# Kernel tuning notes

Measured on AMD Instinct MI355X. Metric: run time of the kernel, lower is better.

Reference implementation:

```python
import jax, jax.numpy as jnp
import numpy as np

# Static multi-scale feature map shapes (value_spatial_shapes) - constants for jit.
SPATIAL = [(128, 128), (64, 64), (32, 32), (16, 16)]
D = 256      # embed_dim
NH = 8       # num_heads
HD = D // NH # head_dim = 32
L = 4        # num_levels
P = 4        # num_points
TP = NH * L * P  # 128 total points


def setup_inputs() -> dict:
    key = jax.random.key(0)
    ks = jax.random.split(key, 10)
    bs, lq = 8, 300
    lv = sum(h * w for h, w in SPATIAL)  # 21760
    s = D ** -0.5
    return {
        "query": jax.random.normal(ks[0], (bs, lq, D), jnp.float32),
        "reference_points": jax.random.uniform(ks[1], (bs, lq, L, 4), jnp.float32),
        "value": jax.random.normal(ks[2], (bs, lv, D), jnp.float32),
        "W_value": jax.random.normal(ks[3], (D, D), jnp.float32) * s,
        "b_value": jnp.zeros((D,), jnp.float32),
        "W_off": jax.random.normal(ks[4], (D, TP * 2), jnp.float32) * (s * 0.01),
        "b_off": jax.random.normal(ks[5], (TP * 2,), jnp.float32) * 0.5,
        "W_attn": jax.random.normal(ks[6], (D, TP), jnp.float32) * (s * 0.01),
        "b_attn": jnp.zeros((TP,), jnp.float32),
        "W_out": jax.random.normal(ks[7], (D, D), jnp.float32) * s,
        "b_out": jnp.zeros((D,), jnp.float32),
    }


def _grid_sample(img, grid):
    """torch F.grid_sample(mode='bilinear', padding_mode='zeros', align_corners=False).
    img: [N, C, H, W]; grid: [N, Hg, Wg, 2] in [-1, 1] (x, y). Returns [N, C, Hg, Wg]."""
    N, C, H, W = img.shape
    gx = (grid[..., 0] + 1.0) * (W * 0.5) - 0.5
    gy = (grid[..., 1] + 1.0) * (H * 0.5) - 0.5
    x0f = jnp.floor(gx)
    y0f = jnp.floor(gy)
    x0 = x0f.astype(jnp.int32)
    y0 = y0f.astype(jnp.int32)
    x1, y1 = x0 + 1, y0 + 1
    wx1 = gx - x0f
    wy1 = gy - y0f
    wx0 = 1.0 - wx1
    wy0 = 1.0 - wy1
    imgf = img.reshape(N, C, H * W)

    def gather(ix, iy):
        valid = (ix >= 0) & (ix < W) & (iy >= 0) & (iy < H)
        idx = jnp.clip(iy, 0, H - 1) * W + jnp.clip(ix, 0, W - 1)
        v = jax.vmap(lambda im, ii: im[:, ii])(imgf, idx)  # [N, C, Hg, Wg]
        return v * valid[:, None, :, :].astype(img.dtype)

    return (gather(x0, y0) * (wx0 * wy0)[:, None]
            + gather(x1, y0) * (wx1 * wy0)[:, None]
            + gather(x0, y1) * (wx0 * wy1)[:, None]
            + gather(x1, y1) * (wx1 * wy1)[:, None])


def reference(query, reference_points, value, W_value, b_value, W_off, b_off,
              W_attn, b_attn, W_out, b_out):
    bs, lq, _ = query.shape
    # value projection + head split
    v = (value @ W_value + b_value).reshape(bs, -1, NH, HD)
    # sampling offsets and attention weights from query
    off = (query @ W_off + b_off).reshape(bs, lq, NH, L, P, 2)
    aw = jax.nn.softmax((query @ W_attn + b_attn).reshape(bs, lq, NH, L * P), axis=-1)
    aw = aw.reshape(bs, lq, NH, L, P)
    # reference_points last dim == 4 branch (cx, cy, w, h)
    ref = reference_points  # [bs, lq, L, 4]
    loc = ref[:, :, None, :, None, :2] + off / P * ref[:, :, None, :, None, 2:] * 0.5
    grids = 2.0 * loc - 1.0  # [bs, lq, NH, L, P, 2]
    # split value per level
    splits = np.cumsum([h * w for h, w in SPATIAL])[:-1]
    v_list = jnp.split(v, splits, axis=1)
    samples = []
    for l, (h, w) in enumerate(SPATIAL):
        img = v_list[l].transpose(0, 2, 3, 1).reshape(bs * NH, HD, h, w)
        g = grids[:, :, :, l].transpose(0, 2, 1, 3, 4).reshape(bs * NH, lq, P, 2)
        samples.append(_grid_sample(img, g))  # [bs*NH, HD, lq, P]
    samp = jnp.stack(samples, axis=-2).reshape(bs * NH, HD, lq, L * P)
    awr = aw.transpose(0, 2, 1, 3, 4).reshape(bs * NH, 1, lq, L * P)
    out = (samp * awr).sum(-1).reshape(bs, NH * HD, lq).transpose(0, 2, 1)
    return out @ W_out + b_out
```

## Files before the change

kernel.cpp:

```cpp
#include <hip/hip_runtime.h>
#include <hip/hip_bf16.h>

typedef short bf16x8 __attribute__((ext_vector_type(8)));
typedef unsigned short u16x8 __attribute__((ext_vector_type(8)));
typedef float f32x4 __attribute__((ext_vector_type(4)));

#define LQ 300
#define LV 21760
#define NQ 2400
#define MROWS 174080

#define VBM 16
#define VGRID 512
#define QBLK 38
#define VNT (MROWS / VBM)

__device__ __forceinline__ unsigned short f2bf(float x) {
    __hip_bfloat16 h = __float2bfloat16(x);
    return *reinterpret_cast<unsigned short*>(&h);
}
__device__ __forceinline__ float bf2f(unsigned short s) {
    return __uint_as_float(((unsigned)s) << 16);
}
__device__ __forceinline__ bf16x8 cvt8(float4 a, float4 b) {
    u16x8 u;
    u[0] = f2bf(a.x); u[1] = f2bf(a.y); u[2] = f2bf(a.z); u[3] = f2bf(a.w);
    u[4] = f2bf(b.x); u[5] = f2bf(b.y); u[6] = f2bf(b.z); u[7] = f2bf(b.w);
    return (bf16x8)u;
}
__device__ __forceinline__ bf16x8 cvt8v(f32x4 a, f32x4 b) {
    u16x8 u;
    u[0] = f2bf(a[0]); u[1] = f2bf(a[1]); u[2] = f2bf(a[2]); u[3] = f2bf(a[3]);
    u[4] = f2bf(b[0]); u[5] = f2bf(b[1]); u[6] = f2bf(b[2]); u[7] = f2bf(b[3]);
    return (bf16x8)u;
}

__global__ void k_wt(const float* __restrict__ Wv, const float* __restrict__ Woff,
                     const float* __restrict__ Wattn, const float* __restrict__ Wout,
                     unsigned short* __restrict__ ws) {
    int i = blockIdx.x * 256 + threadIdx.x;
    if (i < 65536) {
        int n = i >> 8, k = i & 255;
        ws[i] = f2bf(Wv[k * 256 + n]);
    } else if (i < 65536 + 98304) {
        int j = i - 65536;
        int n = j >> 8, k = j & 255;
        float s = (n < 256) ? Woff[k * 256 + n] : Wattn[k * 128 + (n - 256)];
        ws[i] = f2bf(s);
    } else {
        int j = i - 163840;
        int n = j >> 8, k = j & 255;
        ws[i] = f2bf(Wout[k * 256 + n]);
    }
}

__global__ __launch_bounds__(256, 2) void k_vgemm(
    const float* __restrict__ A, const unsigned short* __restrict__ Bt,
    const float* __restrict__ bias, unsigned short* __restrict__ V,
    const float* __restrict__ Q, const unsigned short* __restrict__ Woa,
    const float* __restrict__ b_off, const float* __restrict__ b_attn,
    float* __restrict__ offattn)
{
    __shared__ __align__(16) float buf[4][VBM * 256];
    const int t = threadIdx.x;
    const int lane = t & 63;
    const int wv = t >> 6;
    const int fr = lane & 15, kg = lane >> 4;

    if (blockIdx.x < QBLK) {
        const int rowBase = blockIdx.x * 64;
        int rr[4];
#pragma unroll
        for (int m = 0; m < 4; ++m) rr[m] = min(rowBase + m * 16 + fr, NQ - 1);

        f32x4 acc[4][6];
#pragma unroll
        for (int m = 0; m < 4; m++)
#pragma unroll
            for (int n = 0; n < 6; n++) { f32x4 z = {0.f, 0.f, 0.f, 0.f}; acc[m][n] = z; }

#pragma unroll
        for (int kk = 0; kk < 8; ++kk) {
            const int kb = kk * 32 + kg * 8;
            bf16x8 a[4];
#pragma unroll
            for (int m = 0; m < 4; ++m) {
                float4 q0 = *(const float4*)(Q + (size_t)rr[m] * 256 + kb);
                float4 q1 = *(const float4*)(Q + (size_t)rr[m] * 256 + kb + 4);
                a[m] = cvt8(q0, q1);
            }
#pragma unroll
            for (int n = 0; n < 6; n++) {
                bf16x8 bb = *(const bf16x8*)(Woa + (size_t)(wv * 96 + n * 16 + fr) * 256 + kb);
#pragma unroll
                for (int m = 0; m < 4; ++m)
                    acc[m][n] = __builtin_amdgcn_mfma_f32_16x16x32_bf16(a[m], bb, acc[m][n], 0, 0, 0);
            }
        }

#pragma unroll
        for (int m = 0; m < 4; m++) {
#pragma unroll
            for (int n = 0; n < 6; n++) {
                int col = wv * 96 + n * 16 + fr;
                float bvv = (col < 256) ? b_off[col] : b_attn[col - 256];
#pragma unroll
                for (int r = 0; r < 4; r++) {
                    int row = rowBase + m * 16 + kg * 4 + r;
                    if (row < NQ) offattn[(size_t)row * 384 + col] = acc[m][n][r] + bvv;
                }
            }
        }
        return;
    }

    bf16x8 bw[8][4];
#pragma unroll
    for (int kk = 0; kk < 8; ++kk)
#pragma unroll
        for (int n = 0; n < 4; ++n)
            bw[kk][n] = *(const bf16x8*)(Bt + (size_t)(wv * 64 + n * 16 + fr) * 256 + kk * 32 + kg * 8);
    float bv[4];
#pragma unroll
    for (int n = 0; n < 4; ++n) bv[n] = bias[wv * 64 + n * 16 + fr];

#define VSTAGE(tile, cb)                                                                  \
    {                                                                                     \
        const char* tb = (const char*)(A + (size_t)(tile) * (VBM * 256));                 \
        _Pragma("unroll")                                                                 \
        for (int i = 0; i < 4; ++i) {                                                     \
            const int r = wv * 4 + i;                                                     \
            __builtin_amdgcn_global_load_lds(                                             \
                (const __attribute__((address_space(1))) void*)                           \
                    (tb + (size_t)r * 1024 + ((lane * 16) ^ ((r & 7) << 4))),             \
                (__attribute__((address_space(3))) void*)&buf[cb][r * 256], 16, 0, 0);    \
        }                                                                                 \
    }

    const int tb0 = (int)blockIdx.x - QBLK;
    VSTAGE(tb0, 0);
    if (tb0 + VGRID < VNT)     VSTAGE(tb0 + VGRID, 1);
    if (tb0 + 2 * VGRID < VNT) VSTAGE(tb0 + 2 * VGRID, 2);

    int cur = 0;
    for (int tile = tb0; tile < VNT; tile += VGRID, cur = (cur + 1) & 3) {
        const int nxt3 = tile + 3 * VGRID;
        if (nxt3 < VNT) VSTAGE(nxt3, (cur + 3) & 3);
        int a = (tile + VGRID < VNT) + (tile + 2 * VGRID < VNT) + (nxt3 < VNT);
        if (a == 3)      asm volatile("s_waitcnt vmcnt(12)" ::: "memory");
        else if (a == 2) asm volatile("s_waitcnt vmcnt(8)" ::: "memory");
        else if (a == 1) asm volatile("s_waitcnt vmcnt(4)" ::: "memory");
        else             asm volatile("s_waitcnt vmcnt(0)" ::: "memory");
        __builtin_amdgcn_s_barrier();

        const float* lp = buf[cur];
        f32x4 acc[4];
#pragma unroll
        for (int n = 0; n < 4; ++n) { f32x4 z = {0.f, 0.f, 0.f, 0.f}; acc[n] = z; }

#pragma unroll
        for (int kk = 0; kk < 8; ++kk) {
            const int bsw = ((kk * 32 + kg * 8) * 4) ^ ((fr & 7) << 4);
            f32x4 af0 = *(const f32x4*)((const char*)(lp + fr * 256) + bsw);
            f32x4 af1 = *(const f32x4*)((const char*)(lp + fr * 256) + (bsw ^ 16));
            bf16x8 aa = cvt8v(af0, af1);
#pragma unroll
            for (int n = 0; n < 4; ++n)
                acc[n] = __builtin_amdgcn_mfma_f32_16x16x32_bf16(aa, bw[kk][n], acc[n], 0, 0, 0);
        }

        __builtin_amdgcn_s_barrier();

        unsigned short* cp = (unsigned short*)buf[cur];
#pragma unroll
        for (int n = 0; n < 4; ++n)
#pragma unroll
            for (int r = 0; r < 4; ++r)
                cp[(kg * 4 + r) * 264 + wv * 64 + n * 16 + fr] = f2bf(acc[n][r] + bv[n]);
        asm volatile("s_waitcnt lgkmcnt(0)" ::: "memory");
        __builtin_amdgcn_sched_barrier(0);
        __builtin_amdgcn_s_barrier();

        unsigned short* ob = V + (size_t)tile * (VBM * 256);
#pragma unroll
        for (int i = 0; i < 2; ++i) {
            const int f = i * 256 + t;
            const int row = f >> 5, col = (f & 31) * 8;
            *(u16x8*)(ob + row * 256 + col) = *(const u16x8*)&cp[row * 264 + col];
        }
        __builtin_amdgcn_s_barrier();
    }
#undef VSTAGE
}

__global__ __launch_bounds__(256) void k_sample(
    const float* __restrict__ refp, const float* __restrict__ offattn,
    const unsigned short* __restrict__ V, unsigned short* __restrict__ att)
{
    __shared__ float aw[2][128], gx[2][128], gy[2][128];
    const int t = threadIdx.x;
    const int jj = t >> 7;
    const int tt = t & 127;
    const int row = blockIdx.x * 2 + jj;
    const int b = row / LQ;
    const float* oa = offattn + (size_t)row * 384;

    {
        float logit = oa[256 + tt];
        float m = logit;
        m = fmaxf(m, __shfl_xor(m, 1));
        m = fmaxf(m, __shfl_xor(m, 2));
        m = fmaxf(m, __shfl_xor(m, 4));
        m = fmaxf(m, __shfl_xor(m, 8));
        float e = __expf(logit - m);
        float s = e;
        s += __shfl_xor(s, 1);
        s += __shfl_xor(s, 2);
        s += __shfl_xor(s, 4);
        s += __shfl_xor(s, 8);
        aw[jj][tt] = e / s;
        const int l = (tt >> 2) & 3;
        const float Wl = (l == 0) ? 128.f : (l == 1) ? 64.f : (l == 2) ? 32.f : 16.f;
        float ox = oa[2 * tt], oy = oa[2 * tt + 1];
        const float* rp = refp + ((size_t)row * 4 + l) * 4;
        gx[jj][tt] = (rp[0] + ox * 0.125f * rp[2]) * Wl - 0.5f;
        gy[jj][tt] = (rp[1] + oy * 0.125f * rp[3]) * Wl - 0.5f;
    }
    __syncthreads();

    const int h = tt >> 4;
    const int ch = h * 32 + (tt & 15) * 2;
    float acc0 = 0.f, acc1 = 0.f;
#pragma unroll 4
    for (int p = 0; p < 16; p++) {
        const int l = p >> 2;
        const int Wl = (l == 0) ? 128 : (l == 1) ? 64 : (l == 2) ? 32 : 16;
        const int S  = (l == 0) ? 0 : (l == 1) ? 16384 : (l == 2) ? 20480 : 21504;
        int pt = h * 16 + p;
        float a  = aw[jj][pt];
        float sx = gx[jj][pt], sy = gy[jj][pt];
        float x0f = floorf(sx), y0f = floorf(sy);
        int   x0 = (int)x0f, y0 = (int)y0f;
        float wx1 = sx - x0f, wy1 = sy - y0f;
        float wx0 = 1.f - wx1, wy0 = 1.f - wy1;
        bool vx0 = (unsigned)x0 < (unsigned)Wl;
        bool vx1 = (unsigned)(x0 + 1) < (unsigned)Wl;
        bool vy0 = (unsigned)y0 < (unsigned)Wl;
        bool vy1 = (unsigned)(y0 + 1) < (unsigned)Wl;
        float p00x = 0.f, p00y = 0.f, p01x = 0.f, p01y = 0.f;
        float p10x = 0.f, p10y = 0.f, p11x = 0.f, p11y = 0.f;
        size_t pixBase = (size_t)b * LV + S;
        if (vy0) {
            size_t rb = (pixBase + (size_t)y0 * Wl) * 256 + ch;
            if (vx0) { unsigned u = *(const unsigned*)(V + rb + (size_t)x0 * 256);
                       p00x = bf2f((unsigned short)u); p00y = bf2f((unsigned short)(u >> 16)); }
            if (vx1) { unsigned u = *(const unsigned*)(V + rb + (size_t)x0 * 256 + 256);
                       p01x = bf2f((unsigned short)u); p01y = bf2f((unsigned short)(u >> 16)); }
        }
        if (vy1) {
            size_t rb = (pixBase + (size_t)(y0 + 1) * Wl) * 256 + ch;
            if (vx0) { unsigned u = *(const unsigned*)(V + rb + (size_t)x0 * 256);
                       p10x = bf2f((unsigned short)u); p10y = bf2f((unsigned short)(u >> 16)); }
            if (vx1) { unsigned u = *(const unsigned*)(V + rb + (size_t)x0 * 256 + 256);
                       p11x = bf2f((unsigned short)u); p11y = bf2f((unsigned short)(u >> 16)); }
        }
        acc0 += a * (wy0 * (wx0 * p00x + wx1 * p01x) + wy1 * (wx0 * p10x + wx1 * p11x));
        acc1 += a * (wy0 * (wx0 * p00y + wx1 * p01y) + wy1 * (wx0 * p10y + wx1 * p11y));
    }
    unsigned short o2[2] = { f2bf(acc0), f2bf(acc1) };
    *(unsigned*)(att + (size_t)row * 256 + ch) = *(const unsigned*)o2;
}

__global__ __launch_bounds__(256) void k_outproj(
    const unsigned short* __restrict__ att, const unsigned short* __restrict__ Wout,
    const float* __restrict__ b_out, float* __restrict__ out)
{
    const int t = threadIdx.x;
    const int lane = t & 63;
    const int wc = t >> 6;
    const int fr = lane & 15, kg = lane >> 4;
    const int rowBase = blockIdx.x * 64;

    f32x4 acc[4][4];
#pragma unroll
    for (int m = 0; m < 4; m++)
#pragma unroll
        for (int n = 0; n < 4; n++) { f32x4 z = {0.f, 0.f, 0.f, 0.f}; acc[m][n] = z; }

#pragma unroll
    for (int kk = 0; kk < 8; ++kk) {
        const int kb = kk * 32 + kg * 8;
        bf16x8 a[4], bb[4];
#pragma unroll
        for (int m = 0; m < 4; m++) {
            int row = min(rowBase + m * 16 + fr, NQ - 1);
            a[m] = *(const bf16x8*)(att + (size_t)row * 256 + kb);
        }
#pragma unroll
        for (int n = 0; n < 4; n++)
            bb[n] = *(const bf16x8*)(Wout + (size_t)(wc * 64 + n * 16 + fr) * 256 + kb);
#pragma unroll
        for (int m = 0; m < 4; m++)
#pragma unroll
            for (int n = 0; n < 4; n++)
                acc[m][n] = __builtin_amdgcn_mfma_f32_16x16x32_bf16(a[m], bb[n], acc[m][n], 0, 0, 0);
    }

#pragma unroll
    for (int m = 0; m < 4; m++) {
#pragma unroll
        for (int n = 0; n < 4; n++) {
            int col = wc * 64 + n * 16 + fr;
            float bvv = b_out[col];
#pragma unroll
            for (int r = 0; r < 4; r++) {
                int row = rowBase + m * 16 + kg * 4 + r;
                if (row < NQ) out[(size_t)row * 256 + col] = acc[m][n][r] + bvv;
            }
        }
    }
}

extern "C" void kernel_launch(void* const* d_in, const int* in_sizes, int n_in,
                              void* d_out, int out_size, void* d_ws, size_t ws_size,
                              hipStream_t stream) {
    const float* query   = (const float*)d_in[0];
    const float* refp    = (const float*)d_in[1];
    const float* value   = (const float*)d_in[2];
    const float* W_value = (const float*)d_in[3];
    const float* b_value = (const float*)d_in[4];
    const float* W_off   = (const float*)d_in[5];
    const float* b_off   = (const float*)d_in[6];
    const float* W_attn  = (const float*)d_in[7];
    const float* b_attn  = (const float*)d_in[8];
    const float* W_out   = (const float*)d_in[9];
    const float* b_out   = (const float*)d_in[10];
    float* out = (float*)d_out;

    unsigned short* wsu   = (unsigned short*)d_ws;
    unsigned short* Wt_v  = wsu;
    unsigned short* Wt_oa = Wt_v + 65536;
    unsigned short* Wt_out= Wt_oa + 98304;
    unsigned short* V     = Wt_out + 65536;
    float* offattn = (float*)(V + (size_t)MROWS * 256);
    unsigned short* att = (unsigned short*)(offattn + (size_t)NQ * 384);

    k_wt<<<896, 256, 0, stream>>>(W_value, W_off, W_attn, W_out, wsu);
    k_vgemm<<<VGRID + QBLK, 256, 0, stream>>>(value, Wt_v, b_value, V,
                                              query, Wt_oa, b_off, b_attn, offattn);
    k_sample<<<NQ / 2, 256, 0, stream>>>(refp, offattn, V, att);
    k_outproj<<<38, 256, 0, stream>>>(att, Wt_out, b_out, out);
}
```

Baseline: 114.6 us.

## Replace LDS-staged value GEMM pipeline with direct register prefetch per wave

```diff
diff --git a/kernel.cpp b/kernel.cpp
--- a/kernel.cpp
+++ b/kernel.cpp
@@ -26,12 +26,6 @@
     u16x8 u;
     u[0] = f2bf(a.x); u[1] = f2bf(a.y); u[2] = f2bf(a.z); u[3] = f2bf(a.w);
     u[4] = f2bf(b.x); u[5] = f2bf(b.y); u[6] = f2bf(b.z); u[7] = f2bf(b.w);
-    return (bf16x8)u;
-}
-__device__ __forceinline__ bf16x8 cvt8v(f32x4 a, f32x4 b) {
-    u16x8 u;
-    u[0] = f2bf(a[0]); u[1] = f2bf(a[1]); u[2] = f2bf(a[2]); u[3] = f2bf(a[3]);
-    u[4] = f2bf(b[0]); u[5] = f2bf(b[1]); u[6] = f2bf(b[2]); u[7] = f2bf(b[3]);
     return (bf16x8)u;
 }
 
@@ -61,7 +55,7 @@
     const float* __restrict__ b_off, const float* __restrict__ b_attn,
     float* __restrict__ offattn)
 {
-    __shared__ __align__(16) float buf[4][VBM * 256];
+    __shared__ unsigned short cscr[4][16 * 68];
     const int t = threadIdx.x;
     const int lane = t & 63;
     const int wv = t >> 6;
@@ -124,73 +118,59 @@
 #pragma unroll
     for (int n = 0; n < 4; ++n) bv[n] = bias[wv * 64 + n * 16 + fr];
 
-#define VSTAGE(tile, cb)                                                                  \
-    {                                                                                     \
-        const char* tb = (const char*)(A + (size_t)(tile) * (VBM * 256));                 \
-        _Pragma("unroll")                                                                 \
-        for (int i = 0; i < 4; ++i) {                                                     \
-            const int r = wv * 4 + i;                                                     \
-            __builtin_amdgcn_global_load_lds(                                             \
-                (const __attribute__((address_space(1))) void*)                           \
-                    (tb + (size_t)r * 1024 + ((lane * 16) ^ ((r & 7) << 4))),             \
-                (__attribute__((address_space(3))) void*)&buf[cb][r * 256], 16, 0, 0);    \
-        }                                                                                 \
-    }
-
+    unsigned short* scr = cscr[wv];
     const int tb0 = (int)blockIdx.x - QBLK;
-    VSTAGE(tb0, 0);
-    if (tb0 + VGRID < VNT)     VSTAGE(tb0 + VGRID, 1);
-    if (tb0 + 2 * VGRID < VNT) VSTAGE(tb0 + 2 * VGRID, 2);
-
-    int cur = 0;
-    for (int tile = tb0; tile < VNT; tile += VGRID, cur = (cur + 1) & 3) {
-        const int nxt3 = tile + 3 * VGRID;
-        if (nxt3 < VNT) VSTAGE(nxt3, (cur + 3) & 3);
-        int a = (tile + VGRID < VNT) + (tile + 2 * VGRID < VNT) + (nxt3 < VNT);
-        if (a == 3)      asm volatile("s_waitcnt vmcnt(12)" ::: "memory");
-        else if (a == 2) asm volatile("s_waitcnt vmcnt(8)" ::: "memory");
-        else if (a == 1) asm volatile("s_waitcnt vmcnt(4)" ::: "memory");
-        else             asm volatile("s_waitcnt vmcnt(0)" ::: "memory");
-        __builtin_amdgcn_s_barrier();
-
-        const float* lp = buf[cur];
+    const int koff = kg * 8;
+
+    float4 ar0[8], ar1[8];
+    {
+        const float* pb = A + ((size_t)VBM * tb0 + fr) * 256 + koff;
+#pragma unroll
+        for (int kk = 0; kk < 4; ++kk) {
+            ar0[kk] = *(const float4*)(pb + kk * 32);
+            ar1[kk] = *(const float4*)(pb + kk * 32 + 4);
+        }
+    }
+
+    for (int tile = tb0; tile < VNT; tile += VGRID) {
+        const int nxt = tile + VGRID;
+        const float* pcur = A + ((size_t)VBM * tile + fr) * 256 + koff;
+        const float* pnxt = A + ((size_t)VBM * nxt + fr) * 256 + koff;
+
         f32x4 acc[4];
 #pragma unroll
         for (int n = 0; n < 4; ++n) { f32x4 z = {0.f, 0.f, 0.f, 0.f}; acc[n] = z; }
 
 #pragma unroll
         for (int kk = 0; kk < 8; ++kk) {
-            const int bsw = ((kk * 32 + kg * 8) * 4) ^ ((fr & 7) << 4);
-            f32x4 af0 = *(const f32x4*)((const char*)(lp + fr * 256) + bsw);
-            f32x4 af1 = *(const f32x4*)((const char*)(lp + fr * 256) + (bsw ^ 16));
-            bf16x8 aa = cvt8v(af0, af1);
+            if (kk < 4) {
+                ar0[kk + 4] = *(const float4*)(pcur + (kk + 4) * 32);
+                ar1[kk + 4] = *(const float4*)(pcur + (kk + 4) * 32 + 4);
+            } else if (nxt < VNT) {
+                ar0[kk - 4] = *(const float4*)(pnxt + (kk - 4) * 32);
+                ar1[kk - 4] = *(const float4*)(pnxt + (kk - 4) * 32 + 4);
+            }
+            bf16x8 aa = cvt8(ar0[kk], ar1[kk]);
 #pragma unroll
             for (int n = 0; n < 4; ++n)
                 acc[n] = __builtin_amdgcn_mfma_f32_16x16x32_bf16(aa, bw[kk][n], acc[n], 0, 0, 0);
         }
 
-        __builtin_amdgcn_s_barrier();
-
-        unsigned short* cp = (unsigned short*)buf[cur];
 #pragma unroll
         for (int n = 0; n < 4; ++n)
 #pragma unroll
             for (int r = 0; r < 4; ++r)
-                cp[(kg * 4 + r) * 264 + wv * 64 + n * 16 + fr] = f2bf(acc[n][r] + bv[n]);
+                scr[(kg * 4 + r) * 68 + n * 16 + fr] = f2bf(acc[n][r] + bv[n]);
         asm volatile("s_waitcnt lgkmcnt(0)" ::: "memory");
-        __builtin_amdgcn_sched_barrier(0);
-        __builtin_amdgcn_s_barrier();
-
-        unsigned short* ob = V + (size_t)tile * (VBM * 256);
-#pragma unroll
-        for (int i = 0; i < 2; ++i) {
-            const int f = i * 256 + t;
-            const int row = f >> 5, col = (f & 31) * 8;
-            *(u16x8*)(ob + row * 256 + col) = *(const u16x8*)&cp[row * 264 + col];
-        }
-        __builtin_amdgcn_s_barrier();
-    }
-#undef VSTAGE
+        {
+            const int row = lane >> 2, c = (lane & 3) * 16;
+            u16x8 v0 = *(const u16x8*)&scr[row * 68 + c];
+            u16x8 v1 = *(const u16x8*)&scr[row * 68 + c + 8];
+            unsigned short* ob = V + ((size_t)VBM * tile + row) * 256 + wv * 64 + c;
+            *(u16x8*)ob = v0;
+            *(u16x8*)(ob + 8) = v1;
+        }
+    }
 }
 
 __global__ __launch_bounds__(256) void k_sample(
```

New measurement: 161.9 us. 41.3% more time.
